# Performance work log

Hardware: AMD Instinct MI355X
Metric: run time of the kernel (lower is better)

The kernel has to match this reference:

```python
import jax, jax.numpy as jnp
import numpy as np

N_EMBD = 1024
HEAD_SIZE = 64
BLOCK_SIZE = 512
BATCH = 4


def setup_inputs() -> dict:
    key = jax.random.key(0)
    ks = jax.random.split(key, 5)
    T = BLOCK_SIZE
    x = jax.random.normal(ks[0], (BATCH, 2 * T - 1, N_EMBD), dtype=jnp.float32)
    scale = 1.0 / np.sqrt(N_EMBD)
    Wk = jax.random.normal(ks[1], (N_EMBD, HEAD_SIZE), dtype=jnp.float32) * scale
    Wv = jax.random.normal(ks[2], (N_EMBD, HEAD_SIZE), dtype=jnp.float32) * scale
    Wq = jax.random.normal(ks[3], (N_EMBD, HEAD_SIZE), dtype=jnp.float32) * scale
    # keyWindowBias in torch has shape (1,1,head_size,block_size); store as (hs, T)
    bias = jax.random.normal(ks[4], (HEAD_SIZE, T), dtype=jnp.float32)
    return {"x": x, "Wk": Wk, "Wv": Wv, "Wq": Wq, "bias": bias}


def reference(x, Wk, Wv, Wq, bias):
    B, S, C = x.shape
    T = (S + 1) // 2  # S == 2*T - 1 (block_size)
    xToPred = x[:, -T:, :]
    # block_layer == 0 path: project full sequence for k, v
    k = jnp.einsum('bsc,cd->bsd', x, Wk)        # [B, 2T-1, hs]
    v = jnp.einsum('bsc,cd->bsd', x, Wv)        # [B, 2T-1, hs]
    q = jnp.einsum('btc,cd->btd', xToPred, Wq)  # [B, T, hs]

    # sliding windows: window w covers positions w..w+T-1 (torch unfold semantics)
    idx = jnp.arange(T)[:, None] + jnp.arange(T)[None, :]  # [T, T]

    k_win = k[:, idx, :] + bias.T[None, None, :, :]  # [B, T, T, hs] + [1,1,T,hs]
    wei = jnp.einsum('bwd,bwtd->bwt', q, k_win)      # [B, T, T]
    wei = jax.nn.softmax(wei, axis=-1)

    v_win = v[:, idx, :]                              # [B, T, T, hs]
    out = jnp.einsum('bwt,bwtd->bwd', wei, v_win)     # [B, T, hs]
    return out
```

## Files before the change

kernel.cpp:

```cpp
#include <hip/hip_runtime.h>
#include <hip/hip_bf16.h>

#define BB 4
#define SS 1023
#define TT 512
#define CC 1024
#define DD 64
#define NROW (BB*SS)

typedef float f4 __attribute__((ext_vector_type(4)));
typedef float f2 __attribute__((ext_vector_type(2)));
typedef short bf16x8 __attribute__((ext_vector_type(8)));
typedef float f32x4 __attribute__((ext_vector_type(4)));
typedef unsigned short us4 __attribute__((ext_vector_type(4)));

__device__ __forceinline__ unsigned split_rtn(float v) {
    const unsigned u  = __builtin_bit_cast(unsigned, v);
    const unsigned r  = u + 0x7FFFu + ((u >> 16) & 1u);
    const unsigned hi = r >> 16;
    const float hif   = __builtin_bit_cast(float, r & 0xFFFF0000u);
    const float res   = v - hif;
    const unsigned u2 = __builtin_bit_cast(unsigned, res);
    const unsigned r2 = u2 + 0x7FFFu + ((u2 >> 16) & 1u);
    return (r2 & 0xFFFF0000u) | hi;
}

__global__ __launch_bounds__(512) void xsplit_kernel(
    const float* __restrict__ x,
    unsigned short* __restrict__ xh,
    unsigned short* __restrict__ xl)
{
    const int idx = blockIdx.x * 512 + threadIdx.x;
    const f4 v = ((const f4*)x)[idx];
    us4 h, l;
#pragma unroll
    for (int j = 0; j < 4; ++j) {
        const unsigned hl = split_rtn(v[j]);
        h[j] = (unsigned short)(hl & 0xFFFFu);
        l[j] = (unsigned short)(hl >> 16);
    }
    ((us4*)xh)[idx] = h;
    ((us4*)xl)[idx] = l;
}

__global__ __launch_bounds__(64) void wsplit_kernel(
    const float* __restrict__ Wk,
    const float* __restrict__ Wv,
    const float* __restrict__ Wq,
    unsigned short* __restrict__ bwh,
    unsigned short* __restrict__ bwl)
{
    const int f    = blockIdx.x;
    const int p    = f >> 7;
    const int rem  = f & 127;
    const int nsub = rem >> 5;
    const int ks   = rem & 31;
    const int lane = threadIdx.x;
    const int quad = lane >> 4, l4 = lane & 15;
    const float* W = (p == 0) ? Wk : (p == 1) ? Wv : Wq;
    const int n = nsub * 16 + l4;

    bf16x8 h, l;
#pragma unroll
    for (int j = 0; j < 8; ++j) {
        const int k = ks * 32 + quad * 8 + j;
        const unsigned hl = split_rtn(W[k * DD + n]);
        h[j] = (short)(hl & 0xFFFFu);
        l[j] = (short)(hl >> 16);
    }
    ((bf16x8*)bwh)[f * 64 + lane] = h;
    ((bf16x8*)bwl)[f * 64 + lane] = l;
}

__global__ __launch_bounds__(64) void proj_mfma_kernel(
    const unsigned short* __restrict__ xh,
    const unsigned short* __restrict__ xl,
    const unsigned short* __restrict__ bwh,
    const unsigned short* __restrict__ bwl,
    float* __restrict__ kT,
    float* __restrict__ vbuf,
    float* __restrict__ qbuf)
{
    const int blk  = blockIdx.x;
    const int p    = blk % 3;
    const int mt   = blk / 3;
    const int bs0  = mt * 16;
    const int lane = threadIdx.x;
    const int quad = lane >> 4, l4 = lane & 15;

    int arow = bs0 + l4; if (arow > NROW - 1) arow = NROW - 1;
    const unsigned short* ahp = xh + (size_t)arow * CC;
    const unsigned short* alp = xl + (size_t)arow * CC;
    const bf16x8* bh = (const bf16x8*)bwh + (size_t)(p * 128) * 64 + lane;
    const bf16x8* bl = (const bf16x8*)bwl + (size_t)(p * 128) * 64 + lane;

    f32x4 acc0 = {0.f,0.f,0.f,0.f}, acc1 = {0.f,0.f,0.f,0.f};
    f32x4 acc2 = {0.f,0.f,0.f,0.f}, acc3 = {0.f,0.f,0.f,0.f};

#pragma unroll 4
    for (int ks = 0; ks < 32; ++ks) {
        const int k0 = ks * 32 + quad * 8;
        const bf16x8 ah = *(const bf16x8*)(ahp + k0);
        const bf16x8 al = *(const bf16x8*)(alp + k0);
        const bf16x8 bh0 = bh[(0 * 32 + ks) * 64];
        const bf16x8 bh1 = bh[(1 * 32 + ks) * 64];
        const bf16x8 bh2 = bh[(2 * 32 + ks) * 64];
        const bf16x8 bh3 = bh[(3 * 32 + ks) * 64];
        const bf16x8 bl0 = bl[(0 * 32 + ks) * 64];
        const bf16x8 bl1 = bl[(1 * 32 + ks) * 64];
        const bf16x8 bl2 = bl[(2 * 32 + ks) * 64];
        const bf16x8 bl3 = bl[(3 * 32 + ks) * 64];

        acc0 = __builtin_amdgcn_mfma_f32_16x16x32_bf16(ah, bh0, acc0, 0, 0, 0);
        acc1 = __builtin_amdgcn_mfma_f32_16x16x32_bf16(ah, bh1, acc1, 0, 0, 0);
        acc2 = __builtin_amdgcn_mfma_f32_16x16x32_bf16(ah, bh2, acc2, 0, 0, 0);
        acc3 = __builtin_amdgcn_mfma_f32_16x16x32_bf16(ah, bh3, acc3, 0, 0, 0);
        acc0 = __builtin_amdgcn_mfma_f32_16x16x32_bf16(ah, bl0, acc0, 0, 0, 0);
        acc1 = __builtin_amdgcn_mfma_f32_16x16x32_bf16(ah, bl1, acc1, 0, 0, 0);
        acc2 = __builtin_amdgcn_mfma_f32_16x16x32_bf16(ah, bl2, acc2, 0, 0, 0);
        acc3 = __builtin_amdgcn_mfma_f32_16x16x32_bf16(ah, bl3, acc3, 0, 0, 0);
        acc0 = __builtin_amdgcn_mfma_f32_16x16x32_bf16(al, bh0, acc0, 0, 0, 0);
        acc1 = __builtin_amdgcn_mfma_f32_16x16x32_bf16(al, bh1, acc1, 0, 0, 0);
        acc2 = __builtin_amdgcn_mfma_f32_16x16x32_bf16(al, bh2, acc2, 0, 0, 0);
        acc3 = __builtin_amdgcn_mfma_f32_16x16x32_bf16(al, bh3, acc3, 0, 0, 0);
        acc0 = __builtin_amdgcn_mfma_f32_16x16x32_bf16(al, bl0, acc0, 0, 0, 0);
        acc1 = __builtin_amdgcn_mfma_f32_16x16x32_bf16(al, bl1, acc1, 0, 0, 0);
        acc2 = __builtin_amdgcn_mfma_f32_16x16x32_bf16(al, bl2, acc2, 0, 0, 0);
        acc3 = __builtin_amdgcn_mfma_f32_16x16x32_bf16(al, bl3, acc3, 0, 0, 0);
    }

#pragma unroll
    for (int nsub = 0; nsub < 4; ++nsub) {
        const f32x4 a = (nsub == 0) ? acc0 : (nsub == 1) ? acc1
                       : (nsub == 2) ? acc2 : acc3;
        const int d = nsub * 16 + l4;
#pragma unroll
        for (int reg = 0; reg < 4; ++reg) {
            const int bs = bs0 + quad * 4 + reg;
            if (bs < NROW) {
                const float val = a[reg];
                if (p == 0) {
                    kT[(size_t)d * NROW + bs] = val;
                } else if (p == 1) {
                    vbuf[(size_t)bs * DD + d] = val;
                } else {
                    const int b = bs / SS, s = bs - b * SS;
                    if (s >= TT - 1)
                        qbuf[((size_t)b * TT + (s - (TT - 1))) * DD + d] = val;
                }
            }
        }
    }
}

__global__ __launch_bounds__(512) void qbias_kernel(
    const float* __restrict__ qbuf,
    const float* __restrict__ bias,
    float* __restrict__ qb)
{
    __shared__ __align__(16) float qsT[DD][4];

    const int tid = threadIdx.x;
    const int blk = blockIdx.x;
    const int b   = blk >> 7;
    const int w0  = (blk & 127) * 4;

    if (tid < 4 * DD) {
        const int m = tid >> 6, dd = tid & 63;
        qsT[dd][m] = qbuf[((size_t)b * TT + w0 + m) * DD + dd];
    }
    __syncthreads();

    const int t = tid;
    f4 acc = {0.f, 0.f, 0.f, 0.f};
#pragma unroll 8
    for (int dd = 0; dd < DD; ++dd) {
        const float bb = bias[dd * TT + t];
        const f4 qv = *(const f4*)&qsT[dd][0];
        acc[0] = fmaf(qv[0], bb, acc[0]);
        acc[1] = fmaf(qv[1], bb, acc[1]);
        acc[2] = fmaf(qv[2], bb, acc[2]);
        acc[3] = fmaf(qv[3], bb, acc[3]);
    }
#pragma unroll
    for (int m = 0; m < 4; ++m)
        qb[((size_t)b * TT + w0 + m) * TT + t] = acc[m];
}

__global__ __launch_bounds__(512) void attn_kernel(
    const float* __restrict__ kT,
    const float* __restrict__ vbuf,
    const float* __restrict__ qbuf,
    const float* __restrict__ qb,
    float* __restrict__ out)
{
    __shared__ __align__(8) float qsT[DD][2];
    __shared__ __align__(8) float weiT[TT][2];
    __shared__ float red[16];
    __shared__ float invs[2];
    __shared__ float partial[8][2][DD];

    const int tid  = threadIdx.x;
    const int lane = tid & 63;
    const int wv   = tid >> 6;
    const int blk  = blockIdx.x;
    const int b    = blk >> 8;
    const int w0   = (blk & 255) * 2;

    if (tid < 2 * DD) {
        const int m = tid >> 6, dd = tid & 63;
        qsT[dd][m] = qbuf[((size_t)b * TT + w0 + m) * DD + dd];
    }
    __syncthreads();

    {
        const int t = tid;
        const float* kcol = kT + (size_t)b * SS + w0 + t;
        const float* qbp  = qb + ((size_t)b * TT + w0) * TT + t;
        float a0 = qbp[0];
        float a1 = qbp[TT];
#pragma unroll 8
        for (int dd = 0; dd < DD; ++dd) {
            const float* kr = kcol + (size_t)dd * NROW;
            const float q0 = qsT[dd][0], q1 = qsT[dd][1];
            a0 = fmaf(q0, kr[0], a0);
            a1 = fmaf(q1, kr[1], a1);
        }
        weiT[t][0] = a0;
        weiT[t][1] = a1;
    }
    __syncthreads();

    {
        const int m = wv >> 2, qt = wv & 3;
        const int tb = qt * 128 + lane;
        float r0 = weiT[tb][m], r1 = weiT[tb + 64][m];
        float mx = fmaxf(r0, r1);
#pragma unroll
        for (int off = 1; off < 64; off <<= 1)
            mx = fmaxf(mx, __shfl_xor(mx, off, 64));
        if (lane == 0) red[wv] = mx;
        __syncthreads();
        mx = fmaxf(fmaxf(red[m * 4], red[m * 4 + 1]),
                   fmaxf(red[m * 4 + 2], red[m * 4 + 3]));
        const float e0 = __expf(r0 - mx), e1 = __expf(r1 - mx);
        weiT[tb][m] = e0;
        weiT[tb + 64][m] = e1;
        float sum = e0 + e1;
#pragma unroll
        for (int off = 1; off < 64; off <<= 1)
            sum += __shfl_xor(sum, off, 64);
        if (lane == 0) red[8 + wv] = sum;
        __syncthreads();
        if (tid < 2)
            invs[tid] = 1.f / (red[8 + tid * 4] + red[9 + tid * 4] +
                               red[10 + tid * 4] + red[11 + tid * 4]);
    }
    __syncthreads();

    {
        const int t0r = wv * 64;
        const float* vb = vbuf + ((size_t)b * SS + w0 + t0r) * DD + lane;
        float p0 = 0.f, p1 = 0.f;
        float v0 = vb[0];
#pragma unroll 4
        for (int t = 0; t < 64; ++t) {
            const float v1 = vb[(size_t)(t + 1) * DD];
            const f2 w2 = *(const f2*)&weiT[t0r + t][0];
            p0 = fmaf(w2[0], v0, p0);
            p1 = fmaf(w2[1], v1, p1);
            v0 = v1;
        }
        partial[wv][0][lane] = p0;
        partial[wv][1][lane] = p1;
    }
    __syncthreads();

    if (tid < 2 * DD) {
        const int m = tid >> 6, dd = tid & 63;
        float o = 0.f;
#pragma unroll
        for (int j = 0; j < 8; ++j) o += partial[j][m][dd];
        out[((size_t)b * TT + w0 + m) * DD + dd] = o * invs[m];
    }
}

extern "C" void kernel_launch(void* const* d_in, const int* in_sizes, int n_in,
                              void* d_out, int out_size, void* d_ws, size_t ws_size,
                              hipStream_t stream) {
    const float* x    = (const float*)d_in[0];
    const float* Wk   = (const float*)d_in[1];
    const float* Wv   = (const float*)d_in[2];
    const float* Wq   = (const float*)d_in[3];
    const float* bias = (const float*)d_in[4];
    float* out = (float*)d_out;

    char* ws = (char*)d_ws;
    float* kT             = (float*)(ws + 0);
    float* vbuf           = (float*)(ws + (2u  << 20));
    float* qbuf           = (float*)(ws + (4u  << 20));
    float* qb             = (float*)(ws + (8u  << 20));
    unsigned short* xh    = (unsigned short*)(ws + (16u << 20));
    unsigned short* xl    = (unsigned short*)(ws + (32u << 20));
    unsigned short* bwh   = (unsigned short*)(ws + (48u << 20));
    unsigned short* bwl   = (unsigned short*)(ws + (52u << 20));

    xsplit_kernel<<<NROW * CC / 4 / 512, 512, 0, stream>>>(x, xh, xl);
    wsplit_kernel<<<384, 64, 0, stream>>>(Wk, Wv, Wq, bwh, bwl);
    proj_mfma_kernel<<<768, 64, 0, stream>>>(xh, xl, bwh, bwl, kT, vbuf, qbuf);
    qbias_kernel<<<BB * TT / 4, 512, 0, stream>>>(qbuf, bias, qb);
    attn_kernel<<<BB * TT / 2, 512, 0, stream>>>(kT, vbuf, qbuf, qb, out);
}
```

Before: 126.0 us.

## Fuse x bf16 split into projection GEMM and halve N per block

Removes the separate xsplit kernel that wrote hi/lo bf16 copies of x to workspace. The projection kernel now reads fp32 x directly and does the split in registers before the MFMAs. Each block now covers only half of the 64 output columns, doubling the grid to 1536 blocks, so each x row tile is reread and resplit by 6 blocks instead of 3. This trades an extra launch and a write-plus-read pass over the split x for redundant conversion ALU work and extra fp32 x traffic, which should mostly hit in cache.

After: 122.3 us. 1.03x faster.

```diff
diff --git a/kernel.cpp b/kernel.cpp
--- a/kernel.cpp
+++ b/kernel.cpp
@@ -12,7 +12,6 @@
 typedef float f2 __attribute__((ext_vector_type(2)));
 typedef short bf16x8 __attribute__((ext_vector_type(8)));
 typedef float f32x4 __attribute__((ext_vector_type(4)));
-typedef unsigned short us4 __attribute__((ext_vector_type(4)));
 
 __device__ __forceinline__ unsigned split_rtn(float v) {
     const unsigned u  = __builtin_bit_cast(unsigned, v);
@@ -25,24 +24,6 @@
     return (r2 & 0xFFFF0000u) | hi;
 }
 
-__global__ __launch_bounds__(512) void xsplit_kernel(
-    const float* __restrict__ x,
-    unsigned short* __restrict__ xh,
-    unsigned short* __restrict__ xl)
-{
-    const int idx = blockIdx.x * 512 + threadIdx.x;
-    const f4 v = ((const f4*)x)[idx];
-    us4 h, l;
-#pragma unroll
-    for (int j = 0; j < 4; ++j) {
-        const unsigned hl = split_rtn(v[j]);
-        h[j] = (unsigned short)(hl & 0xFFFFu);
-        l[j] = (unsigned short)(hl >> 16);
-    }
-    ((us4*)xh)[idx] = h;
-    ((us4*)xl)[idx] = l;
-}
-
 __global__ __launch_bounds__(64) void wsplit_kernel(
     const float* __restrict__ Wk,
     const float* __restrict__ Wv,
@@ -73,8 +54,7 @@
 }
 
 __global__ __launch_bounds__(64) void proj_mfma_kernel(
-    const unsigned short* __restrict__ xh,
-    const unsigned short* __restrict__ xl,
+    const float* __restrict__ x,
     const unsigned short* __restrict__ bwh,
     const unsigned short* __restrict__ bwl,
     float* __restrict__ kT,
@@ -82,58 +62,61 @@
     float* __restrict__ qbuf)
 {
     const int blk  = blockIdx.x;
-    const int p    = blk % 3;
-    const int mt   = blk / 3;
+    const int nh   = blk & 1;
+    const int pm   = blk >> 1;
+    const int p    = pm % 3;
+    const int mt   = pm / 3;
     const int bs0  = mt * 16;
     const int lane = threadIdx.x;
     const int quad = lane >> 4, l4 = lane & 15;
+    const int nsub0 = nh * 2;
 
     int arow = bs0 + l4; if (arow > NROW - 1) arow = NROW - 1;
-    const unsigned short* ahp = xh + (size_t)arow * CC;
-    const unsigned short* alp = xl + (size_t)arow * CC;
-    const bf16x8* bh = (const bf16x8*)bwh + (size_t)(p * 128) * 64 + lane;
-    const bf16x8* bl = (const bf16x8*)bwl + (size_t)(p * 128) * 64 + lane;
+    const float* ap = x + (size_t)arow * CC;
+    const bf16x8* bh = (const bf16x8*)bwh
+                     + (size_t)((p * 4 + nsub0) * 32) * 64 + lane;
+    const bf16x8* bl = (const bf16x8*)bwl
+                     + (size_t)((p * 4 + nsub0) * 32) * 64 + lane;
 
     f32x4 acc0 = {0.f,0.f,0.f,0.f}, acc1 = {0.f,0.f,0.f,0.f};
-    f32x4 acc2 = {0.f,0.f,0.f,0.f}, acc3 = {0.f,0.f,0.f,0.f};
 
 #pragma unroll 4
     for (int ks = 0; ks < 32; ++ks) {
         const int k0 = ks * 32 + quad * 8;
-        const bf16x8 ah = *(const bf16x8*)(ahp + k0);
-        const bf16x8 al = *(const bf16x8*)(alp + k0);
+        const f4 xa = *(const f4*)(ap + k0);
+        const f4 xb = *(const f4*)(ap + k0 + 4);
+        bf16x8 ah, al;
+#pragma unroll
+        for (int j = 0; j < 4; ++j) {
+            const unsigned hl = split_rtn(xa[j]);
+            ah[j] = (short)(hl & 0xFFFFu);
+            al[j] = (short)(hl >> 16);
+        }
+#pragma unroll
+        for (int j = 0; j < 4; ++j) {
+            const unsigned hl = split_rtn(xb[j]);
+            ah[4 + j] = (short)(hl & 0xFFFFu);
+            al[4 + j] = (short)(hl >> 16);
+        }
         const bf16x8 bh0 = bh[(0 * 32 + ks) * 64];
         const bf16x8 bh1 = bh[(1 * 32 + ks) * 64];
-        const bf16x8 bh2 = bh[(2 * 32 + ks) * 64];
-        const bf16x8 bh3 = bh[(3 * 32 + ks) * 64];
         const bf16x8 bl0 = bl[(0 * 32 + ks) * 64];
         const bf16x8 bl1 = bl[(1 * 32 + ks) * 64];
-        const bf16x8 bl2 = bl[(2 * 32 + ks) * 64];
-        const bf16x8 bl3 = bl[(3 * 32 + ks) * 64];
 
         acc0 = __builtin_amdgcn_mfma_f32_16x16x32_bf16(ah, bh0, acc0, 0, 0, 0);
         acc1 = __builtin_amdgcn_mfma_f32_16x16x32_bf16(ah, bh1, acc1, 0, 0, 0);
-        acc2 = __builtin_amdgcn_mfma_f32_16x16x32_bf16(ah, bh2, acc2, 0, 0, 0);
-        acc3 = __builtin_amdgcn_mfma_f32_16x16x32_bf16(ah, bh3, acc3, 0, 0, 0);
         acc0 = __builtin_amdgcn_mfma_f32_16x16x32_bf16(ah, bl0, acc0, 0, 0, 0);
         acc1 = __builtin_amdgcn_mfma_f32_16x16x32_bf16(ah, bl1, acc1, 0, 0, 0);
-        acc2 = __builtin_amdgcn_mfma_f32_16x16x32_bf16(ah, bl2, acc2, 0, 0, 0);
-        acc3 = __builtin_amdgcn_mfma_f32_16x16x32_bf16(ah, bl3, acc3, 0, 0, 0);
         acc0 = __builtin_amdgcn_mfma_f32_16x16x32_bf16(al, bh0, acc0, 0, 0, 0);
         acc1 = __builtin_amdgcn_mfma_f32_16x16x32_bf16(al, bh1, acc1, 0, 0, 0);
-        acc2 = __builtin_amdgcn_mfma_f32_16x16x32_bf16(al, bh2, acc2, 0, 0, 0);
-        acc3 = __builtin_amdgcn_mfma_f32_16x16x32_bf16(al, bh3, acc3, 0, 0, 0);
         acc0 = __builtin_amdgcn_mfma_f32_16x16x32_bf16(al, bl0, acc0, 0, 0, 0);
         acc1 = __builtin_amdgcn_mfma_f32_16x16x32_bf16(al, bl1, acc1, 0, 0, 0);
-        acc2 = __builtin_amdgcn_mfma_f32_16x16x32_bf16(al, bl2, acc2, 0, 0, 0);
-        acc3 = __builtin_amdgcn_mfma_f32_16x16x32_bf16(al, bl3, acc3, 0, 0, 0);
-    }
-
-#pragma unroll
-    for (int nsub = 0; nsub < 4; ++nsub) {
-        const f32x4 a = (nsub == 0) ? acc0 : (nsub == 1) ? acc1
-                       : (nsub == 2) ? acc2 : acc3;
-        const int d = nsub * 16 + l4;
+    }
+
+#pragma unroll
+    for (int s = 0; s < 2; ++s) {
+        const f32x4 a = s ? acc1 : acc0;
+        const int d = (nsub0 + s) * 16 + l4;
 #pragma unroll
         for (int reg = 0; reg < 4; ++reg) {
             const int bs = bs0 + quad * 4 + reg;
@@ -144,9 +127,9 @@
                 } else if (p == 1) {
                     vbuf[(size_t)bs * DD + d] = val;
                 } else {
-                    const int b = bs / SS, s = bs - b * SS;
-                    if (s >= TT - 1)
-                        qbuf[((size_t)b * TT + (s - (TT - 1))) * DD + d] = val;
+                    const int b = bs / SS, ss = bs - b * SS;
+                    if (ss >= TT - 1)
+                        qbuf[((size_t)b * TT + (ss - (TT - 1))) * DD + d] = val;
                 }
             }
         }
@@ -300,14 +283,11 @@
     float* vbuf           = (float*)(ws + (2u  << 20));
     float* qbuf           = (float*)(ws + (4u  << 20));
     float* qb             = (float*)(ws + (8u  << 20));
-    unsigned short* xh    = (unsigned short*)(ws + (16u << 20));
-    unsigned short* xl    = (unsigned short*)(ws + (32u << 20));
-    unsigned short* bwh   = (unsigned short*)(ws + (48u << 20));
-    unsigned short* bwl   = (unsigned short*)(ws + (52u << 20));
-
-    xsplit_kernel<<<NROW * CC / 4 / 512, 512, 0, stream>>>(x, xh, xl);
+    unsigned short* bwh   = (unsigned short*)(ws + (16u << 20));
+    unsigned short* bwl   = (unsigned short*)(ws + (20u << 20));
+
     wsplit_kernel<<<384, 64, 0, stream>>>(Wk, Wv, Wq, bwh, bwl);
-    proj_mfma_kernel<<<768, 64, 0, stream>>>(xh, xl, bwh, bwl, kT, vbuf, qbuf);
+    proj_mfma_kernel<<<1536, 64, 0, stream>>>(x, bwh, bwl, kT, vbuf, qbuf);
     qbias_kernel<<<BB * TT / 4, 512, 0, stream>>>(qbuf, bias, qb);
     attn_kernel<<<BB * TT / 2, 512, 0, stream>>>(kT, vbuf, qbuf, qb, out);
 }
```
